# Optimization experiments

Measured on AMD Instinct MI355X. Metric: run time of the kernel, lower is better.

The kernel has to match this reference:

```python
import jax, jax.numpy as jnp
import numpy as np

BS, T, LAB, DEMO, HID, F = 1024, 128, 64, 16, 32, 4


def setup_inputs() -> dict:
    key = jax.random.key(0)
    ks = jax.random.split(key, 12)
    s = 0.1
    return {
        "x": jax.random.normal(ks[0], (BS, T, LAB), dtype=jnp.float32),
        "static": jax.random.normal(ks[1], (BS, DEMO), dtype=jnp.float32),
        "demo_W": jax.random.normal(ks[2], (HID, DEMO), dtype=jnp.float32) * s,
        "demo_b": jax.random.normal(ks[3], (HID,), dtype=jnp.float32) * s,
        "lab_W": jax.random.normal(ks[4], (LAB, LAB), dtype=jnp.float32) * s,
        "lab_b": jax.random.normal(ks[5], (LAB,), dtype=jnp.float32) * s,
        # per-lab GRU weights stacked over lab_dim; input size is 1 so W_ih is [LAB, 3F]
        "Wih": jax.random.normal(ks[6], (LAB, 3 * F), dtype=jnp.float32) * 0.5,
        "bih": jax.random.normal(ks[7], (LAB, 3 * F), dtype=jnp.float32) * 0.5,
        "Whh": jax.random.normal(ks[8], (LAB, 3 * F, F), dtype=jnp.float32) * 0.5,
        "bhh": jax.random.normal(ks[9], (LAB, 3 * F), dtype=jnp.float32) * 0.5,
        "out_W": jax.random.normal(ks[10], (HID, LAB * F + HID), dtype=jnp.float32) * s,
        "out_b": jax.random.normal(ks[11], (HID,), dtype=jnp.float32) * s,
    }


def reference(x, static, demo_W, demo_b, lab_W, lab_b, Wih, bih, Whh, bhh, out_W, out_b):
    bs, t, lab = x.shape
    f = Whh.shape[-1]
    demo = static @ demo_W.T + demo_b                     # [bs, HID]
    xp = x @ lab_W.T + lab_b                              # [bs, T, LAB]

    def step(h, x_t):
        # h: [bs, LAB, F], x_t: [bs, LAB] (scalar input per lab-GRU)
        gi = x_t[:, :, None] * Wih[None] + bih[None]      # [bs, LAB, 3F]
        gh = jnp.einsum('blf,lgf->blg', h, Whh) + bhh[None]
        r = jax.nn.sigmoid(gi[..., :f] + gh[..., :f])
        z = jax.nn.sigmoid(gi[..., f:2 * f] + gh[..., f:2 * f])
        n = jnp.tanh(gi[..., 2 * f:] + r * gh[..., 2 * f:])
        h_new = (1.0 - z) * n + z * h
        return h_new, None

    h0 = jnp.zeros((bs, lab, f), dtype=x.dtype)
    h_last, _ = jax.lax.scan(step, h0, jnp.swapaxes(xp, 0, 1))  # only final step is used
    feat = h_last.reshape(bs, lab * f)                     # [bs, LAB*F]
    cat = jnp.concatenate([demo, feat], axis=-1)
    return cat @ out_W.T + out_b                           # [bs, HID]
```

## Files before the change

kernel.cpp:

```cpp
#include <hip/hip_runtime.h>
#include <cstddef>

#define BSZ   1024
#define TT    128
#define LAB   64
#define DEMO  16
#define HID   32
#define FF    4
#define CHUNK 32
#define NCHUNK (TT / CHUNK)

__device__ __forceinline__ float sig_s(float pre_scaled) {
    return __builtin_amdgcn_rcpf(1.0f + __builtin_amdgcn_exp2f(pre_scaled));
}
__device__ __forceinline__ float tanh_s(float y_scaled) {
    return fmaf(-2.0f, __builtin_amdgcn_rcpf(__builtin_amdgcn_exp2f(y_scaled) + 1.0f), 1.0f);
}

__global__ __launch_bounds__(64, 1)
void mcgru_fused(const float* __restrict__ x,
                 const float* __restrict__ stat,
                 const float* __restrict__ demo_W,
                 const float* __restrict__ demo_b,
                 const float* __restrict__ lab_W,
                 const float* __restrict__ lab_b,
                 const float* __restrict__ Wih,
                 const float* __restrict__ bih,
                 const float* __restrict__ Whh,
                 const float* __restrict__ bhh,
                 const float* __restrict__ out_W,
                 const float* __restrict__ out_b,
                 float* __restrict__ out)
{
    const int b = blockIdx.x;
    const int l = threadIdx.x;

    __shared__ float xs[2][CHUNK * LAB];
    __shared__ float cat[HID + LAB * FF];

    const float S1 = -1.442695041f;
    const float S2 =  2.885390082f;

    float wl[LAB];
    #pragma unroll
    for (int k = 0; k < LAB; k += 4) {
        float4 v = *reinterpret_cast<const float4*>(lab_W + l * LAB + k);
        wl[k] = v.x; wl[k+1] = v.y; wl[k+2] = v.z; wl[k+3] = v.w;
    }
    float whh[48];
    #pragma unroll
    for (int k = 0; k < 48; k += 4) {
        float4 v = *reinterpret_cast<const float4*>(Whh + l * 48 + k);
        whh[k] = v.x; whh[k+1] = v.y; whh[k+2] = v.z; whh[k+3] = v.w;
    }
    float wih[12], bihv[12], bhhv[12];
    #pragma unroll
    for (int k = 0; k < 12; k += 4) {
        float4 a = *reinterpret_cast<const float4*>(Wih + l * 12 + k);
        float4 c = *reinterpret_cast<const float4*>(bih + l * 12 + k);
        float4 d = *reinterpret_cast<const float4*>(bhh + l * 12 + k);
        wih[k] = a.x; wih[k+1] = a.y; wih[k+2] = a.z; wih[k+3] = a.w;
        bihv[k] = c.x; bihv[k+1] = c.y; bihv[k+2] = c.z; bihv[k+3] = c.w;
        bhhv[k] = d.x; bhhv[k+1] = d.y; bhhv[k+2] = d.z; bhhv[k+3] = d.w;
    }
    float bc[8];
    #pragma unroll
    for (int g = 0; g < 8; ++g) {
        bc[g]  = S1 * (bihv[g] + bhhv[g]);
        wih[g] *= S1;
        #pragma unroll
        for (int k = 0; k < 4; ++k) whh[g*4 + k] *= S1;
    }
    #pragma unroll
    for (int g = 8; g < 12; ++g) {
        wih[g]  *= S2;
        bihv[g] *= S2;
        bhhv[g] *= S2;
        #pragma unroll
        for (int k = 0; k < 4; ++k) whh[g*4 + k] *= S2;
    }
    const float lb = lab_b[l];

    float h0 = 0.f, h1 = 0.f, h2 = 0.f, h3 = 0.f;

    const float4* xrow4 = reinterpret_cast<const float4*>(x + (size_t)b * TT * LAB);

    #pragma unroll
    for (int i = 0; i < 8; ++i) {
        float4 v = xrow4[i * 64 + l];
        *reinterpret_cast<float4*>(&xs[0][(i * 64 + l) * 4]) = v;
    }
    __syncthreads();

    for (int c = 0; c < NCHUNK; ++c) {
        const int cur = c & 1, nxt = cur ^ 1;
        const bool more = (c + 1 < NCHUNK);

        float4 stage[8];
        if (more) {
            const float4* src = xrow4 + (c + 1) * (CHUNK * LAB / 4);
            #pragma unroll
            for (int i = 0; i < 8; ++i) stage[i] = src[i * 64 + l];
        }

        #pragma unroll 2
        for (int t = 0; t < CHUNK; ++t) {
            const float4* row = reinterpret_cast<const float4*>(&xs[cur][t * LAB]);
            float a0 = 0.f, a1 = 0.f, a2 = 0.f, a3 = 0.f;
            #pragma unroll
            for (int k = 0; k < LAB / 4; ++k) {
                float4 v = row[k];
                a0 = fmaf(v.x, wl[4*k + 0], a0);
                a1 = fmaf(v.y, wl[4*k + 1], a1);
                a2 = fmaf(v.z, wl[4*k + 2], a2);
                a3 = fmaf(v.w, wl[4*k + 3], a3);
            }
            const float xt = lb + ((a0 + a1) + (a2 + a3));

            float pre[8];
            #pragma unroll
            for (int g = 0; g < 8; ++g) {
                float acc = fmaf(xt, wih[g], bc[g]);
                acc = fmaf(h0, whh[g*4 + 0], acc);
                acc = fmaf(h1, whh[g*4 + 1], acc);
                acc = fmaf(h2, whh[g*4 + 2], acc);
                acc = fmaf(h3, whh[g*4 + 3], acc);
                pre[g] = acc;
            }
            const float r0 = sig_s(pre[0]);
            const float r1 = sig_s(pre[1]);
            const float r2 = sig_s(pre[2]);
            const float r3 = sig_s(pre[3]);
            const float z0 = sig_s(pre[4]);
            const float z1 = sig_s(pre[5]);
            const float z2 = sig_s(pre[6]);
            const float z3 = sig_s(pre[7]);

            float ghn[4], gin[4];
            #pragma unroll
            for (int i = 0; i < 4; ++i) {
                const int g = 8 + i;
                float acc = bhhv[g];
                acc = fmaf(h0, whh[g*4 + 0], acc);
                acc = fmaf(h1, whh[g*4 + 1], acc);
                acc = fmaf(h2, whh[g*4 + 2], acc);
                acc = fmaf(h3, whh[g*4 + 3], acc);
                ghn[i] = acc;
                gin[i] = fmaf(xt, wih[g], bihv[g]);
            }
            const float n0 = tanh_s(fmaf(r0, ghn[0], gin[0]));
            const float n1 = tanh_s(fmaf(r1, ghn[1], gin[1]));
            const float n2 = tanh_s(fmaf(r2, ghn[2], gin[2]));
            const float n3 = tanh_s(fmaf(r3, ghn[3], gin[3]));

            h0 = fmaf(z0, h0 - n0, n0);
            h1 = fmaf(z1, h1 - n1, n1);
            h2 = fmaf(z2, h2 - n2, n2);
            h3 = fmaf(z3, h3 - n3, n3);
        }

        if (more) {
            #pragma unroll
            for (int i = 0; i < 8; ++i)
                *reinterpret_cast<float4*>(&xs[nxt][(i * 64 + l) * 4]) = stage[i];
            __syncthreads();
        }
    }

    cat[HID + l*4 + 0] = h0;
    cat[HID + l*4 + 1] = h1;
    cat[HID + l*4 + 2] = h2;
    cat[HID + l*4 + 3] = h3;
    if (l < HID) {
        float acc = demo_b[l];
        const float* sr = stat + (size_t)b * DEMO;
        const float* dwr = demo_W + l * DEMO;
        #pragma unroll
        for (int d = 0; d < DEMO; ++d)
            acc = fmaf(sr[d], dwr[d], acc);
        cat[l] = acc;
    }
    __syncthreads();

    if (l < HID) {
        float acc = out_b[l];
        const float* wrow = out_W + l * (HID + LAB * FF);
        #pragma unroll
        for (int i = 0; i < HID + LAB * FF; i += 4) {
            float4 wv = *reinterpret_cast<const float4*>(wrow + i);
            acc = fmaf(cat[i + 0], wv.x, acc);
            acc = fmaf(cat[i + 1], wv.y, acc);
            acc = fmaf(cat[i + 2], wv.z, acc);
            acc = fmaf(cat[i + 3], wv.w, acc);
        }
        out[(size_t)b * HID + l] = acc;
    }
}

extern "C" void kernel_launch(void* const* d_in, const int* in_sizes, int n_in,
                              void* d_out, int out_size, void* d_ws, size_t ws_size,
                              hipStream_t stream) {
    const float* x      = (const float*)d_in[0];
    const float* stat   = (const float*)d_in[1];
    const float* demo_W = (const float*)d_in[2];
    const float* demo_b = (const float*)d_in[3];
    const float* lab_W  = (const float*)d_in[4];
    const float* lab_b  = (const float*)d_in[5];
    const float* Wih    = (const float*)d_in[6];
    const float* bih    = (const float*)d_in[7];
    const float* Whh    = (const float*)d_in[8];
    const float* bhh    = (const float*)d_in[9];
    const float* out_W  = (const float*)d_in[10];
    const float* out_b  = (const float*)d_in[11];
    float* out = (float*)d_out;

    dim3 grid(BSZ);
    dim3 block(LAB);
    hipLaunchKernelGGL(mcgru_fused, grid, block, 0, stream,
                       x, stat, demo_W, demo_b, lab_W, lab_b,
                       Wih, bih, Whh, bhh, out_W, out_b, out);
}
```

Before: 168.1 us.

## Split lab projection into a separate GEMM kernel feeding the GRU recurrence

Moves the x @ lab_W projection out of the serial GRU loop into its own kernel. That kernel writes the projected inputs to workspace in a [b, lab, t] layout, so each GRU thread can stream its own contiguous time series as float4 loads with one-step prefetch. This takes the 64-FMA dot product and the shared-memory reads off the per-timestep critical path of the latency-bound recurrence. The cost is a second launch and an extra round trip of the 32 MB intermediate through global memory.

```diff
diff --git a/kernel.cpp b/kernel.cpp
--- a/kernel.cpp
+++ b/kernel.cpp
@@ -7,46 +7,81 @@
 #define DEMO  16
 #define HID   32
 #define FF    4
-#define CHUNK 32
-#define NCHUNK (TT / CHUNK)
-
-__device__ __forceinline__ float sig_s(float pre_scaled) {
-    return __builtin_amdgcn_rcpf(1.0f + __builtin_amdgcn_exp2f(pre_scaled));
-}
-__device__ __forceinline__ float tanh_s(float y_scaled) {
-    return fmaf(-2.0f, __builtin_amdgcn_rcpf(__builtin_amdgcn_exp2f(y_scaled) + 1.0f), 1.0f);
+
+__device__ __forceinline__ float sig_s(float p) {
+    return __builtin_amdgcn_rcpf(1.0f + __builtin_amdgcn_exp2f(p));
+}
+__device__ __forceinline__ float tanh_s(float y) {
+    return fmaf(-2.0f, __builtin_amdgcn_rcpf(__builtin_amdgcn_exp2f(y) + 1.0f), 1.0f);
+}
+
+__global__ __launch_bounds__(128)
+void proj_gemm(const float* __restrict__ x,
+               const float* __restrict__ lab_W,
+               const float* __restrict__ lab_b,
+               float* __restrict__ xp)
+{
+    const int b = blockIdx.x;
+    const int t = threadIdx.x;
+
+    __shared__ float wls[LAB * LAB];
+    __shared__ float lbs[LAB];
+
+    {
+        const float4* src = reinterpret_cast<const float4*>(lab_W);
+        float4* dst = reinterpret_cast<float4*>(wls);
+        #pragma unroll
+        for (int i = 0; i < 8; ++i) dst[i * 128 + t] = src[i * 128 + t];
+        if (t < LAB) lbs[t] = lab_b[t];
+    }
+
+    float xr[LAB];
+    const float4* xr4 = reinterpret_cast<const float4*>(x + ((size_t)b * TT + t) * LAB);
+    #pragma unroll
+    for (int k = 0; k < 16; ++k) {
+        float4 v = xr4[k];
+        xr[4*k] = v.x; xr[4*k+1] = v.y; xr[4*k+2] = v.z; xr[4*k+3] = v.w;
+    }
+    __syncthreads();
+
+    float* xpb = xp + (size_t)b * LAB * TT;
+    #pragma unroll 2
+    for (int l = 0; l < LAB; ++l) {
+        const float4* w4 = reinterpret_cast<const float4*>(wls + l * LAB);
+        float a0 = 0.f, a1 = 0.f, a2 = 0.f, a3 = 0.f;
+        #pragma unroll
+        for (int k = 0; k < 16; ++k) {
+            float4 w = w4[k];
+            a0 = fmaf(w.x, xr[4*k + 0], a0);
+            a1 = fmaf(w.y, xr[4*k + 1], a1);
+            a2 = fmaf(w.z, xr[4*k + 2], a2);
+            a3 = fmaf(w.w, xr[4*k + 3], a3);
+        }
+        xpb[l * TT + t] = lbs[l] + ((a0 + a1) + (a2 + a3));
+    }
 }
 
 __global__ __launch_bounds__(64, 1)
-void mcgru_fused(const float* __restrict__ x,
-                 const float* __restrict__ stat,
-                 const float* __restrict__ demo_W,
-                 const float* __restrict__ demo_b,
-                 const float* __restrict__ lab_W,
-                 const float* __restrict__ lab_b,
-                 const float* __restrict__ Wih,
-                 const float* __restrict__ bih,
-                 const float* __restrict__ Whh,
-                 const float* __restrict__ bhh,
-                 const float* __restrict__ out_W,
-                 const float* __restrict__ out_b,
-                 float* __restrict__ out)
+void gru_kernel(const float* __restrict__ xp,
+                const float* __restrict__ stat,
+                const float* __restrict__ demo_W,
+                const float* __restrict__ demo_b,
+                const float* __restrict__ Wih,
+                const float* __restrict__ bih,
+                const float* __restrict__ Whh,
+                const float* __restrict__ bhh,
+                const float* __restrict__ out_W,
+                const float* __restrict__ out_b,
+                float* __restrict__ out)
 {
     const int b = blockIdx.x;
     const int l = threadIdx.x;
 
-    __shared__ float xs[2][CHUNK * LAB];
     __shared__ float cat[HID + LAB * FF];
 
     const float S1 = -1.442695041f;
     const float S2 =  2.885390082f;
 
-    float wl[LAB];
-    #pragma unroll
-    for (int k = 0; k < LAB; k += 4) {
-        float4 v = *reinterpret_cast<const float4*>(lab_W + l * LAB + k);
-        wl[k] = v.x; wl[k+1] = v.y; wl[k+2] = v.z; wl[k+3] = v.w;
-    }
     float whh[48];
     #pragma unroll
     for (int k = 0; k < 48; k += 4) {
@@ -79,43 +114,21 @@
         #pragma unroll
         for (int k = 0; k < 4; ++k) whh[g*4 + k] *= S2;
     }
-    const float lb = lab_b[l];
 
     float h0 = 0.f, h1 = 0.f, h2 = 0.f, h3 = 0.f;
 
-    const float4* xrow4 = reinterpret_cast<const float4*>(x + (size_t)b * TT * LAB);
-
-    #pragma unroll
-    for (int i = 0; i < 8; ++i) {
-        float4 v = xrow4[i * 64 + l];
-        *reinterpret_cast<float4*>(&xs[0][(i * 64 + l) * 4]) = v;
-    }
-    __syncthreads();
-
-    for (int c = 0; c < NCHUNK; ++c) {
-        const int cur = c & 1, nxt = cur ^ 1;
-        const bool more = (c + 1 < NCHUNK);
-
-        float4 stage[8];
-        if (more) {
-            const float4* src = xrow4 + (c + 1) * (CHUNK * LAB / 4);
-            #pragma unroll
-            for (int i = 0; i < 8; ++i) stage[i] = src[i * 64 + l];
-        }
-
-        #pragma unroll 2
-        for (int t = 0; t < CHUNK; ++t) {
-            const float4* row = reinterpret_cast<const float4*>(&xs[cur][t * LAB]);
-            float a0 = 0.f, a1 = 0.f, a2 = 0.f, a3 = 0.f;
-            #pragma unroll
-            for (int k = 0; k < LAB / 4; ++k) {
-                float4 v = row[k];
-                a0 = fmaf(v.x, wl[4*k + 0], a0);
-                a1 = fmaf(v.y, wl[4*k + 1], a1);
-                a2 = fmaf(v.z, wl[4*k + 2], a2);
-                a3 = fmaf(v.w, wl[4*k + 3], a3);
-            }
-            const float xt = lb + ((a0 + a1) + (a2 + a3));
+    const float4* xq = reinterpret_cast<const float4*>(xp + ((size_t)b * LAB + l) * TT);
+    float4 xcur = xq[0];
+
+    #pragma unroll 1
+    for (int tb = 0; tb < TT / 4; ++tb) {
+        float4 xnxt;
+        if (tb + 1 < TT / 4) xnxt = xq[tb + 1];
+
+        float xts[4] = {xcur.x, xcur.y, xcur.z, xcur.w};
+        #pragma unroll
+        for (int j = 0; j < 4; ++j) {
+            const float xt = xts[j];
 
             float pre[8];
             #pragma unroll
@@ -158,13 +171,7 @@
             h2 = fmaf(z2, h2 - n2, n2);
             h3 = fmaf(z3, h3 - n3, n3);
         }
-
-        if (more) {
-            #pragma unroll
-            for (int i = 0; i < 8; ++i)
-                *reinterpret_cast<float4*>(&xs[nxt][(i * 64 + l) * 4]) = stage[i];
-            __syncthreads();
-        }
+        xcur = xnxt;
     }
 
     cat[HID + l*4 + 0] = h0;
@@ -214,9 +221,10 @@
     const float* out_b  = (const float*)d_in[11];
     float* out = (float*)d_out;
 
-    dim3 grid(BSZ);
-    dim3 block(LAB);
-    hipLaunchKernelGGL(mcgru_fused, grid, block, 0, stream,
-                       x, stat, demo_W, demo_b, lab_W, lab_b,
-                       Wih, bih, Whh, bhh, out_W, out_b, out);
-}
+    float* xp = (float*)d_ws;
+
+    hipLaunchKernelGGL(proj_gemm, dim3(BSZ), dim3(128), 0, stream,
+                       x, lab_W, lab_b, xp);
+    hipLaunchKernelGGL(gru_kernel, dim3(BSZ), dim3(LAB), 0, stream,
+                       xp, stat, demo_W, demo_b, Wih, bih, Whh, bhh, out_W, out_b, out);
+}
```

After: 189.2 us. 1.13x slower.
